# Kernel tuning notes

Measured on AMD Instinct MI355X. Metric: run time of the kernel, lower is better.

The kernel has to match this reference:

```python
import jax, jax.numpy as jnp
import numpy as np

N = 25000      # nodes
E = 400000     # edges
IN = 1024      # in_channels
FC = 128       # feature_channels
ADD = 20       # additional_channels
MID = (FC + ADD) // 4   # 37, fc1 output (heads=4)
OUT = 3
EPS = 1e-5
NEG_SLOPE = 0.01


def setup_inputs() -> dict:
    key = jax.random.key(0)
    ks = jax.random.split(key, 16)
    d = {}
    d["features"] = jax.random.normal(ks[0], (N, IN), dtype=jnp.float32)
    d["edges"] = jax.random.randint(ks[1], (2, E), 0, N, dtype=jnp.int64)
    d["edges2"] = jax.random.randint(ks[2], (2, 1000), 0, N, dtype=jnp.int64)
    d["edge_features"] = jax.random.normal(ks[3], (E, 1), dtype=jnp.float32)
    d["additional_feature"] = jax.random.normal(ks[4], (N, ADD), dtype=jnp.float32)
    # SAGEConv params: lin_l (neighbor path, with bias), lin_r (root path, no bias)
    s = 1.0 / np.sqrt(IN)
    d["Wl"] = jax.random.uniform(ks[5], (FC, IN), jnp.float32, -s, s)
    d["bl"] = jax.random.uniform(ks[6], (FC,), jnp.float32, -s, s)
    d["Wr"] = jax.random.uniform(ks[7], (FC, IN), jnp.float32, -s, s)
    s1 = 1.0 / np.sqrt(FC + ADD)
    d["W1"] = jax.random.uniform(ks[8], (MID, FC + ADD), jnp.float32, -s1, s1)
    d["b1"] = jax.random.uniform(ks[9], (MID,), jnp.float32, -s1, s1)
    s2 = 1.0 / np.sqrt(MID)
    d["W2"] = jax.random.uniform(ks[10], (OUT, MID), jnp.float32, -s2, s2)
    d["b2"] = jax.random.uniform(ks[11], (OUT,), jnp.float32, -s2, s2)
    # BatchNorm1d (eval mode -> running stats)
    d["gamma"] = jnp.ones((MID,), jnp.float32)
    d["beta"] = jnp.zeros((MID,), jnp.float32)
    d["run_mean"] = jax.random.normal(ks[12], (MID,), dtype=jnp.float32) * 0.1
    d["run_var"] = jnp.abs(jax.random.normal(ks[13], (MID,), dtype=jnp.float32)) * 0.1 + 1.0
    return d


def reference(features, edges, edges2, edge_features, additional_feature,
              Wl, bl, Wr, W1, b1, W2, b2, gamma, beta, run_mean, run_var):
    src, dst = edges[0], edges[1]  # PyG: messages flow source -> target
    # scatter-mean of neighbor features onto targets
    agg = jax.ops.segment_sum(features[src], dst, num_segments=N)        # [N, IN]
    deg = jax.ops.segment_sum(jnp.ones((E,), features.dtype), dst, num_segments=N)
    agg = agg / jnp.maximum(deg, 1.0)[:, None]
    # SAGEConv: lin_l(mean_neigh) + lin_r(x)
    x = agg @ Wl.T + bl + features @ Wr.T                                 # [N, FC]
    x = jnp.where(x >= 0, x, NEG_SLOPE * x)                               # leaky_relu
    # dropout is identity in eval mode
    x = jnp.concatenate([x, additional_feature], axis=1) @ W1.T + b1      # [N, MID]
    x = jnp.maximum(x, 0.0)                                               # relu
    x = gamma * (x - run_mean) * jax.lax.rsqrt(run_var + EPS) + beta      # BN eval
    return x @ W2.T + b2                                                  # [N, OUT]
```

## Files before the change

### kernel.cpp

```cpp
#include <hip/hip_runtime.h>

#define N_NODES 25000
#define N_EDGES 400000
#define IN_CH 1024
#define FC 128
#define ADD_CH 20
#define XCH 148
#define MID 37
#define OUT_CH 3
#define MAXDEG 64
#define NG16 1564

typedef short bf16x8 __attribute__((ext_vector_type(8)));
typedef float f32x4 __attribute__((ext_vector_type(4)));

__device__ __forceinline__ unsigned int f2bf(float x) {
    unsigned int u = __builtin_bit_cast(unsigned int, x);
    unsigned int lsb = (u >> 16) & 1u;
    u += 0x7fffu + lsb;
    return u >> 16;
}
__device__ __forceinline__ unsigned int pkbf(float a, float b) {
    return f2bf(a) | (f2bf(b) << 16);
}
__device__ __forceinline__ float bflo(unsigned int v) {
    return __builtin_bit_cast(float, v << 16);
}
__device__ __forceinline__ float bfhi(unsigned int v) {
    return __builtin_bit_cast(float, v & 0xffff0000u);
}

#define WSWZ_B 16
#define BUILD_B 1563

__global__ __launch_bounds__(256) void prep_kernel(const float* __restrict__ Wl,
                                                   const float* __restrict__ Wr,
                                                   const float* __restrict__ A,
                                                   const int* __restrict__ edges,
                                                   ushort* __restrict__ Wpk,
                                                   ushort* __restrict__ Fpk,
                                                   int* __restrict__ cursor,
                                                   int* __restrict__ col) {
    int b = blockIdx.x, t = threadIdx.x;
    if (b < WSWZ_B) {
        int w = t >> 6, lane = t & 63, l15 = lane & 15, q8 = (lane >> 4) * 8;
        int ch = b * 16 + l15;
        const float* src = (ch < FC) ? (Wl + (size_t)ch * IN_CH)
                                     : (Wr + (size_t)(ch - FC) * IN_CH);
        #pragma unroll
        for (int j = 0; j < 8; ++j) {
            int kt = w * 8 + j;
            float4 lo = *(const float4*)(src + kt * 32 + q8);
            float4 hi = *(const float4*)(src + kt * 32 + q8 + 4);
            uint4 pk;
            pk.x = pkbf(lo.x, lo.y); pk.y = pkbf(lo.z, lo.w);
            pk.z = pkbf(hi.x, hi.y); pk.w = pkbf(hi.z, hi.w);
            ((uint4*)Wpk)[(size_t)(b * 32 + kt) * 64 + lane] = pk;
        }
    } else if (b < WSWZ_B + NG16) {
        int g16 = b - WSWZ_B;
        int w = t >> 6, lane = t & 63, l15 = lane & 15, q8 = (lane >> 4) * 8;
        int row = g16 * 16 + l15;
        if (row >= N_NODES) row = N_NODES - 1;
        const float* src = A + (size_t)row * IN_CH;
        #pragma unroll
        for (int j = 0; j < 8; ++j) {
            int kt = w * 8 + j;
            float4 lo = *(const float4*)(src + kt * 32 + q8);
            float4 hi = *(const float4*)(src + kt * 32 + q8 + 4);
            uint4 pk;
            pk.x = pkbf(lo.x, lo.y); pk.y = pkbf(lo.z, lo.w);
            pk.z = pkbf(hi.x, hi.y); pk.w = pkbf(hi.z, hi.w);
            ((uint4*)Fpk)[(size_t)(g16 * 32 + kt) * 64 + lane] = pk;
        }
    } else {
        int e = (b - WSWZ_B - NG16) * 256 + t;
        if (e < N_EDGES) {
            int dst = edges[N_EDGES + e];
            int pos = atomicAdd(&cursor[dst], 1);
            if (pos < MAXDEG) col[dst * MAXDEG + pos] = edges[e];
        }
    }
}

__global__ __launch_bounds__(256, 4) void gemm_kernel(const ushort* __restrict__ Wpk,
                                                      const ushort* __restrict__ Fpk,
                                                      ushort* __restrict__ Py,
                                                      ushort* __restrict__ Pz) {
    int t = threadIdx.x, w = t >> 6, lane = t & 63;
    int l15 = lane & 15, q = lane >> 4;
    int bb = blockIdx.x, m0 = bb * 32;
    const bf16x8* Wf = (const bf16x8*)Wpk + (size_t)(w * 4) * 32 * 64 + lane;
    const bf16x8* Ff = (const bf16x8*)Fpk + (size_t)(bb * 2) * 32 * 64 + lane;
    f32x4 acc[4][2] = {};
    bf16x8 a0[4], a1[4], bA[2], bB[2];
    #pragma unroll
    for (int cf = 0; cf < 4; ++cf) a0[cf] = Wf[(size_t)cf * 32 * 64];
    #pragma unroll
    for (int g = 0; g < 2; ++g) bA[g] = Ff[(size_t)g * 32 * 64];
    for (int kt = 0; kt < 32; kt += 2) {
        #pragma unroll
        for (int cf = 0; cf < 4; ++cf) a1[cf] = Wf[(size_t)(cf * 32 + kt + 1) * 64];
        #pragma unroll
        for (int g = 0; g < 2; ++g) bB[g] = Ff[(size_t)(g * 32 + kt + 1) * 64];
        #pragma unroll
        for (int cf = 0; cf < 4; ++cf) {
            acc[cf][0] = __builtin_amdgcn_mfma_f32_16x16x32_bf16(a0[cf], bA[0], acc[cf][0], 0, 0, 0);
            acc[cf][1] = __builtin_amdgcn_mfma_f32_16x16x32_bf16(a0[cf], bA[1], acc[cf][1], 0, 0, 0);
        }
        if (kt + 2 < 32) {
            #pragma unroll
            for (int cf = 0; cf < 4; ++cf) a0[cf] = Wf[(size_t)(cf * 32 + kt + 2) * 64];
            #pragma unroll
            for (int g = 0; g < 2; ++g) bA[g] = Ff[(size_t)(g * 32 + kt + 2) * 64];
        }
        #pragma unroll
        for (int cf = 0; cf < 4; ++cf) {
            acc[cf][0] = __builtin_amdgcn_mfma_f32_16x16x32_bf16(a1[cf], bB[0], acc[cf][0], 0, 0, 0);
            acc[cf][1] = __builtin_amdgcn_mfma_f32_16x16x32_bf16(a1[cf], bB[1], acc[cf][1], 0, 0, 0);
        }
    }
    #pragma unroll
    for (int g = 0; g < 2; ++g) {
        int node = m0 + g * 16 + l15;
        if (node < N_NODES) {
            ushort* base = (w < 2) ? (Py + (size_t)node * FC + w * 64)
                                   : (Pz + (size_t)node * FC + (w - 2) * 64);
            #pragma unroll
            for (int cf = 0; cf < 4; ++cf) {
                f32x4 v = acc[cf][g];
                uint2 pk;
                pk.x = pkbf(v[0], v[1]);
                pk.y = pkbf(v[2], v[3]);
                *(uint2*)(base + cf * 16 + q * 4) = pk;
            }
        }
    }
}

__global__ __launch_bounds__(256) void fused_tail(const ushort* __restrict__ Py,
                                                  const ushort* __restrict__ Pz,
                                                  const int* __restrict__ deg,
                                                  const int* __restrict__ col,
                                                  const float* __restrict__ addf,
                                                  const float* __restrict__ bl,
                                                  const float* __restrict__ W1,
                                                  const float* __restrict__ b1,
                                                  const float* __restrict__ W2,
                                                  const float* __restrict__ b2,
                                                  const float* __restrict__ gamma,
                                                  const float* __restrict__ beta,
                                                  const float* __restrict__ rmean,
                                                  const float* __restrict__ rvar,
                                                  float* __restrict__ out) {
    __shared__ float W1s[XCH][MID + 3];
    __shared__ float xbuf[4][XCH + 4];
    __shared__ float hbuf[4][MID + 3];
    int t = threadIdx.x;
    for (int idx = t; idx < MID * XCH; idx += 256) {
        int j = idx / XCH, k = idx - j * XCH;
        W1s[k][j] = W1[idx];
    }
    __syncthreads();
    int w = t >> 6, lane = t & 63;
    int n = blockIdx.x * 4 + w;
    bool valid = (n < N_NODES);
    int d = valid ? deg[n] : 0;
    if (d > MAXDEG) d = MAXDEG;
    int g = lane >> 4, c16 = lane & 15;
    float s[8] = {0.f, 0.f, 0.f, 0.f, 0.f, 0.f, 0.f, 0.f};
    if (d > 0) {
        int cidx = col[n * MAXDEG + (lane < d ? lane : 0)];
        for (int i = 0; i < d; i += 8) {
            int e0 = i + g, e1 = i + g + 4;
            int s0 = __shfl(cidx, (e0 < d) ? e0 : 0);
            int s1 = __shfl(cidx, (e1 < d) ? e1 : 0);
            uint4 v0 = *(const uint4*)&Py[(size_t)s0 * FC + c16 * 8];
            uint4 v1 = *(const uint4*)&Py[(size_t)s1 * FC + c16 * 8];
            if (e0 < d) {
                s[0] += bflo(v0.x); s[1] += bfhi(v0.x);
                s[2] += bflo(v0.y); s[3] += bfhi(v0.y);
                s[4] += bflo(v0.z); s[5] += bfhi(v0.z);
                s[6] += bflo(v0.w); s[7] += bfhi(v0.w);
            }
            if (e1 < d) {
                s[0] += bflo(v1.x); s[1] += bfhi(v1.x);
                s[2] += bflo(v1.y); s[3] += bfhi(v1.y);
                s[4] += bflo(v1.z); s[5] += bfhi(v1.z);
                s[6] += bflo(v1.w); s[7] += bfhi(v1.w);
            }
        }
        #pragma unroll
        for (int r = 0; r < 8; ++r) {
            s[r] += __shfl_xor(s[r], 16);
            s[r] += __shfl_xor(s[r], 32);
        }
    }
    if (valid) {
        if (lane < 16) {
            #pragma unroll
            for (int r = 0; r < 8; ++r) xbuf[w][lane * 8 + r] = s[r];
        }
        float invd = 1.0f / (float)(d > 1 ? d : 1);
        unsigned int vr = *(const unsigned int*)&Pz[(size_t)n * FC + lane * 2];
        float x0 = xbuf[w][2 * lane] * invd + bl[2 * lane] + bflo(vr);
        float x1 = xbuf[w][2 * lane + 1] * invd + bl[2 * lane + 1] + bfhi(vr);
        x0 = (x0 >= 0.f) ? x0 : 0.01f * x0;
        x1 = (x1 >= 0.f) ? x1 : 0.01f * x1;
        xbuf[w][2 * lane] = x0;
        xbuf[w][2 * lane + 1] = x1;
        if (lane < ADD_CH) xbuf[w][FC + lane] = addf[(size_t)n * ADD_CH + lane];
        if (lane < MID) {
            float h = b1[lane];
            #pragma unroll 4
            for (int k = 0; k < XCH; ++k) h += W1s[k][lane] * xbuf[w][k];
            h = fmaxf(h, 0.0f);
            h = gamma[lane] * (h - rmean[lane]) * rsqrtf(rvar[lane] + 1e-5f) + beta[lane];
            hbuf[w][lane] = h;
        }
        if (lane < OUT_CH) {
            float o = b2[lane];
            #pragma unroll
            for (int j = 0; j < MID; ++j) o += W2[lane * MID + j] * hbuf[w][j];
            out[(size_t)n * OUT_CH + lane] = o;
        }
    }
}


extern "C" void kernel_launch(void* const* d_in, const int* in_sizes, int n_in,
                              void* d_out, int out_size, void* d_ws, size_t ws_size,
                              hipStream_t stream) {
    const float* features = (const float*)d_in[0];
    const int*   edges    = (const int*)d_in[1];
    const float* addf     = (const float*)d_in[4];
    const float* Wl       = (const float*)d_in[5];
    const float* bl       = (const float*)d_in[6];
    const float* Wr       = (const float*)d_in[7];
    const float* W1       = (const float*)d_in[8];
    const float* b1       = (const float*)d_in[9];
    const float* W2       = (const float*)d_in[10];
    const float* b2       = (const float*)d_in[11];
    const float* gamma    = (const float*)d_in[12];
    const float* beta     = (const float*)d_in[13];
    const float* rmean    = (const float*)d_in[14];
    const float* rvar     = (const float*)d_in[15];
    float* out = (float*)d_out;

    char* ws = (char*)d_ws;
    size_t off = 0;
    ushort* Py = (ushort*)(ws + off);     off += (size_t)N_NODES * FC * 2;
    ushort* Pz = (ushort*)(ws + off);     off += (size_t)N_NODES * FC * 2;
    ushort* Wpk = (ushort*)(ws + off);    off += (size_t)16 * 32 * 64 * 16;
    int* cursor = (int*)(ws + off);       off += (size_t)N_NODES * 4;
    int* col = (int*)(ws + off);          off += (size_t)N_NODES * MAXDEG * 4;
    ushort* Fpk = (ushort*)(ws + off);    off += (size_t)NG16 * 32 * 64 * 16;

    (void)hipMemsetAsync(cursor, 0, (size_t)N_NODES * 4, stream);

    prep_kernel<<<WSWZ_B + NG16 + BUILD_B, 256, 0, stream>>>(Wl, Wr, features, edges,
                                                             Wpk, Fpk, cursor, col);

    gemm_kernel<<<(N_NODES + 31) / 32, 256, 0, stream>>>(Wpk, Fpk, Py, Pz);

    fused_tail<<<(N_NODES + 3) / 4, 256, 0, stream>>>(Py, Pz, cursor, col, addf, bl,
                                                      W1, b1, W2, b2, gamma, beta,
                                                      rmean, rvar, out);
}
```

Before: 290.4 us.

## Fuse feature bf16 conversion into GEMM via LDS staging, unroll gather loads

Drops the separate pass that converted the fp32 feature matrix into a packed bf16 buffer in global memory. The GEMM kernel now reads fp32 features directly, converts them and stages them in shared memory before running the MFMA loop, which removes one full write and re-read of a 51 MB intermediate. The tail gather is also unrolled to issue four neighbor loads per iteration instead of two, giving more memory-level parallelism. The costs are 64 KB of LDS per GEMM block, which limits occupancy, and a simpler prefetch scheme for the weight fragments.

After: 299.1 us. 1.03x slower.

```diff
diff --git a/kernel.cpp b/kernel.cpp
--- a/kernel.cpp
+++ b/kernel.cpp
@@ -9,7 +9,6 @@
 #define MID 37
 #define OUT_CH 3
 #define MAXDEG 64
-#define NG16 1564
 
 typedef short bf16x8 __attribute__((ext_vector_type(8)));
 typedef float f32x4 __attribute__((ext_vector_type(4)));
@@ -35,10 +34,8 @@
 
 __global__ __launch_bounds__(256) void prep_kernel(const float* __restrict__ Wl,
                                                    const float* __restrict__ Wr,
-                                                   const float* __restrict__ A,
                                                    const int* __restrict__ edges,
                                                    ushort* __restrict__ Wpk,
-                                                   ushort* __restrict__ Fpk,
                                                    int* __restrict__ cursor,
                                                    int* __restrict__ col) {
     int b = blockIdx.x, t = threadIdx.x;
@@ -57,24 +54,8 @@
             pk.z = pkbf(hi.x, hi.y); pk.w = pkbf(hi.z, hi.w);
             ((uint4*)Wpk)[(size_t)(b * 32 + kt) * 64 + lane] = pk;
         }
-    } else if (b < WSWZ_B + NG16) {
-        int g16 = b - WSWZ_B;
-        int w = t >> 6, lane = t & 63, l15 = lane & 15, q8 = (lane >> 4) * 8;
-        int row = g16 * 16 + l15;
-        if (row >= N_NODES) row = N_NODES - 1;
-        const float* src = A + (size_t)row * IN_CH;
-        #pragma unroll
-        for (int j = 0; j < 8; ++j) {
-            int kt = w * 8 + j;
-            float4 lo = *(const float4*)(src + kt * 32 + q8);
-            float4 hi = *(const float4*)(src + kt * 32 + q8 + 4);
-            uint4 pk;
-            pk.x = pkbf(lo.x, lo.y); pk.y = pkbf(lo.z, lo.w);
-            pk.z = pkbf(hi.x, hi.y); pk.w = pkbf(hi.z, hi.w);
-            ((uint4*)Fpk)[(size_t)(g16 * 32 + kt) * 64 + lane] = pk;
-        }
     } else {
-        int e = (b - WSWZ_B - NG16) * 256 + t;
+        int e = (b - WSWZ_B) * 256 + t;
         if (e < N_EDGES) {
             int dst = edges[N_EDGES + e];
             int pos = atomicAdd(&cursor[dst], 1);
@@ -83,42 +64,56 @@
     }
 }
 
-__global__ __launch_bounds__(256, 4) void gemm_kernel(const ushort* __restrict__ Wpk,
-                                                      const ushort* __restrict__ Fpk,
-                                                      ushort* __restrict__ Py,
-                                                      ushort* __restrict__ Pz) {
+__global__ __launch_bounds__(256) void gemm_kernel(const float* __restrict__ A,
+                                                   const ushort* __restrict__ Wpk,
+                                                   ushort* __restrict__ Py,
+                                                   ushort* __restrict__ Pz) {
+    __shared__ __align__(16) ushort Fs[2 * 32 * 64 * 8];
     int t = threadIdx.x, w = t >> 6, lane = t & 63;
     int l15 = lane & 15, q = lane >> 4;
-    int bb = blockIdx.x, m0 = bb * 32;
+    int m0 = blockIdx.x * 32;
+
     const bf16x8* Wf = (const bf16x8*)Wpk + (size_t)(w * 4) * 32 * 64 + lane;
-    const bf16x8* Ff = (const bf16x8*)Fpk + (size_t)(bb * 2) * 32 * 64 + lane;
+    bf16x8 aw[4], an[4];
+    #pragma unroll
+    for (int cf = 0; cf < 4; ++cf) aw[cf] = Wf[(size_t)cf * 32 * 64];
+
+    {
+        int r = t >> 3;
+        int p0 = t & 7;
+        int row = m0 + r; if (row >= N_NODES) row = N_NODES - 1;
+        const float* src = A + (size_t)row * IN_CH;
+        int g = r >> 4, l = r & 15;
+        #pragma unroll
+        for (int m = 0; m < 16; ++m) {
+            int o = m * 8 + p0;
+            int kt = o >> 2, qq = o & 3;
+            float4 lo = *(const float4*)(src + o * 8);
+            float4 hi = *(const float4*)(src + o * 8 + 4);
+            uint4 pk;
+            pk.x = pkbf(lo.x, lo.y); pk.y = pkbf(lo.z, lo.w);
+            pk.z = pkbf(hi.x, hi.y); pk.w = pkbf(hi.z, hi.w);
+            *(uint4*)&Fs[(size_t)((g * 32 + kt) * 64 + qq * 16 + l) * 8] = pk;
+        }
+    }
+    __syncthreads();
+
+    const bf16x8* Ff = (const bf16x8*)Fs + lane;
     f32x4 acc[4][2] = {};
-    bf16x8 a0[4], a1[4], bA[2], bB[2];
-    #pragma unroll
-    for (int cf = 0; cf < 4; ++cf) a0[cf] = Wf[(size_t)cf * 32 * 64];
-    #pragma unroll
-    for (int g = 0; g < 2; ++g) bA[g] = Ff[(size_t)g * 32 * 64];
-    for (int kt = 0; kt < 32; kt += 2) {
-        #pragma unroll
-        for (int cf = 0; cf < 4; ++cf) a1[cf] = Wf[(size_t)(cf * 32 + kt + 1) * 64];
-        #pragma unroll
-        for (int g = 0; g < 2; ++g) bB[g] = Ff[(size_t)(g * 32 + kt + 1) * 64];
+    for (int kt = 0; kt < 32; ++kt) {
+        if (kt + 1 < 32) {
+            #pragma unroll
+            for (int cf = 0; cf < 4; ++cf) an[cf] = Wf[(size_t)(cf * 32 + kt + 1) * 64];
+        }
+        bf16x8 b0 = Ff[(size_t)(0 * 32 + kt) * 64];
+        bf16x8 b1 = Ff[(size_t)(1 * 32 + kt) * 64];
         #pragma unroll
         for (int cf = 0; cf < 4; ++cf) {
-            acc[cf][0] = __builtin_amdgcn_mfma_f32_16x16x32_bf16(a0[cf], bA[0], acc[cf][0], 0, 0, 0);
-            acc[cf][1] = __builtin_amdgcn_mfma_f32_16x16x32_bf16(a0[cf], bA[1], acc[cf][1], 0, 0, 0);
-        }
-        if (kt + 2 < 32) {
-            #pragma unroll
-            for (int cf = 0; cf < 4; ++cf) a0[cf] = Wf[(size_t)(cf * 32 + kt + 2) * 64];
-            #pragma unroll
-            for (int g = 0; g < 2; ++g) bA[g] = Ff[(size_t)(g * 32 + kt + 2) * 64];
-        }
-        #pragma unroll
-        for (int cf = 0; cf < 4; ++cf) {
-            acc[cf][0] = __builtin_amdgcn_mfma_f32_16x16x32_bf16(a1[cf], bB[0], acc[cf][0], 0, 0, 0);
-            acc[cf][1] = __builtin_amdgcn_mfma_f32_16x16x32_bf16(a1[cf], bB[1], acc[cf][1], 0, 0, 0);
-        }
+            acc[cf][0] = __builtin_amdgcn_mfma_f32_16x16x32_bf16(aw[cf], b0, acc[cf][0], 0, 0, 0);
+            acc[cf][1] = __builtin_amdgcn_mfma_f32_16x16x32_bf16(aw[cf], b1, acc[cf][1], 0, 0, 0);
+        }
+        #pragma unroll
+        for (int cf = 0; cf < 4; ++cf) aw[cf] = an[cf];
     }
     #pragma unroll
     for (int g = 0; g < 2; ++g) {
@@ -171,23 +166,25 @@
     float s[8] = {0.f, 0.f, 0.f, 0.f, 0.f, 0.f, 0.f, 0.f};
     if (d > 0) {
         int cidx = col[n * MAXDEG + (lane < d ? lane : 0)];
-        for (int i = 0; i < d; i += 8) {
-            int e0 = i + g, e1 = i + g + 4;
-            int s0 = __shfl(cidx, (e0 < d) ? e0 : 0);
-            int s1 = __shfl(cidx, (e1 < d) ? e1 : 0);
-            uint4 v0 = *(const uint4*)&Py[(size_t)s0 * FC + c16 * 8];
-            uint4 v1 = *(const uint4*)&Py[(size_t)s1 * FC + c16 * 8];
-            if (e0 < d) {
-                s[0] += bflo(v0.x); s[1] += bfhi(v0.x);
-                s[2] += bflo(v0.y); s[3] += bfhi(v0.y);
-                s[4] += bflo(v0.z); s[5] += bfhi(v0.z);
-                s[6] += bflo(v0.w); s[7] += bfhi(v0.w);
+        for (int i = 0; i < d; i += 16) {
+            int e[4];
+            uint4 v[4];
+            #pragma unroll
+            for (int j = 0; j < 4; ++j) {
+                int ee = i + g + j * 4;
+                e[j] = __shfl(cidx, (ee < d) ? ee : 0);
             }
-            if (e1 < d) {
-                s[0] += bflo(v1.x); s[1] += bfhi(v1.x);
-                s[2] += bflo(v1.y); s[3] += bfhi(v1.y);
-                s[4] += bflo(v1.z); s[5] += bfhi(v1.z);
-                s[6] += bflo(v1.w); s[7] += bfhi(v1.w);
+            #pragma unroll
+            for (int j = 0; j < 4; ++j)
+                v[j] = *(const uint4*)&Py[(size_t)e[j] * FC + c16 * 8];
+            #pragma unroll
+            for (int j = 0; j < 4; ++j) {
+                if (i + g + j * 4 < d) {
+                    s[0] += bflo(v[j].x); s[1] += bfhi(v[j].x);
+                    s[2] += bflo(v[j].y); s[3] += bfhi(v[j].y);
+                    s[4] += bflo(v[j].z); s[5] += bfhi(v[j].z);
+                    s[6] += bflo(v[j].w); s[7] += bfhi(v[j].w);
+                }
             }
         }
         #pragma unroll
@@ -254,14 +251,12 @@
     ushort* Wpk = (ushort*)(ws + off);    off += (size_t)16 * 32 * 64 * 16;
     int* cursor = (int*)(ws + off);       off += (size_t)N_NODES * 4;
     int* col = (int*)(ws + off);          off += (size_t)N_NODES * MAXDEG * 4;
-    ushort* Fpk = (ushort*)(ws + off);    off += (size_t)NG16 * 32 * 64 * 16;
 
     (void)hipMemsetAsync(cursor, 0, (size_t)N_NODES * 4, stream);
 
-    prep_kernel<<<WSWZ_B + NG16 + BUILD_B, 256, 0, stream>>>(Wl, Wr, features, edges,
-                                                             Wpk, Fpk, cursor, col);
-
-    gemm_kernel<<<(N_NODES + 31) / 32, 256, 0, stream>>>(Wpk, Fpk, Py, Pz);
+    prep_kernel<<<WSWZ_B + BUILD_B, 256, 0, stream>>>(Wl, Wr, edges, Wpk, cursor, col);
+
+    gemm_kernel<<<(N_NODES + 31) / 32, 256, 0, stream>>>(features, Wpk, Py, Pz);
 
     fused_tail<<<(N_NODES + 3) / 4, 256, 0, stream>>>(Py, Pz, cursor, col, addf, bl,
                                                       W1, b1, W2, b2, gamma, beta,
```
